# Kernel tuning notes

Hardware: AMD Instinct MI355X
Metric: run time of the kernel (lower is better)

The kernel has to match this reference:

```python
import jax, jax.numpy as jnp
import numpy as np

N_NODES = 50000
N_EDGES = 1600000
IN_DIM = 256
HID = 128
BATCH = 16384
EDGE_FEAT = 6
BN_EPS = 1e-5


def _glorot(key, shape):
    fan_in, fan_out = shape[0], shape[1]
    lim = float(np.sqrt(6.0 / (fan_in + fan_out)))
    return jax.random.uniform(key, shape, jnp.float32, -lim, lim)


def setup_inputs() -> dict:
    key = jax.random.key(0)
    ks = jax.random.split(key, 20)
    return {
        "x": jax.random.normal(ks[0], (N_NODES, IN_DIM), jnp.float32),
        "edge_index": jax.random.randint(ks[1], (2, N_EDGES), 0, N_NODES, jnp.int64 if jax.config.jax_enable_x64 else jnp.int32),
        "src_nodes": jax.random.randint(ks[2], (BATCH,), 0, N_NODES),
        "tgt_nodes": jax.random.randint(ks[3], (BATCH,), 0, N_NODES),
        "edge_features": jax.random.uniform(ks[4], (BATCH, EDGE_FEAT), jnp.float32),
        # SAGEConv layer 0: lin_l (aggregated neighbors, has bias), lin_r (root, no bias)
        "sage_wl0": _glorot(ks[5], (IN_DIM, HID)),
        "sage_b0": jnp.zeros((HID,), jnp.float32),
        "sage_wr0": _glorot(ks[6], (IN_DIM, HID)),
        # SAGEConv layer 1
        "sage_wl1": _glorot(ks[7], (HID, HID)),
        "sage_b1": jnp.zeros((HID,), jnp.float32),
        "sage_wr1": _glorot(ks[8], (HID, HID)),
        # edge_processor: Linear(6, 64)
        "ep_w": _glorot(ks[9], (EDGE_FEAT, HID // 2)),
        "ep_b": jnp.zeros((HID // 2,), jnp.float32),
        # predictor: Linear(320,128) -> ReLU -> BN(128) -> Linear(128,64) -> ReLU -> Linear(64,1) -> Sigmoid
        "p1_w": _glorot(ks[10], (2 * HID + HID // 2, HID)),
        "p1_b": jnp.zeros((HID,), jnp.float32),
        "bn_gamma": jnp.ones((HID,), jnp.float32),
        "bn_beta": jnp.zeros((HID,), jnp.float32),
        "bn_mean": jnp.zeros((HID,), jnp.float32),
        "bn_var": jnp.ones((HID,), jnp.float32),
        "p2_w": _glorot(ks[11], (HID, HID // 2)),
        "p2_b": jnp.zeros((HID // 2,), jnp.float32),
        "p3_w": _glorot(ks[12], (HID // 2, 1)),
        "p3_b": jnp.zeros((1,), jnp.float32),
    }


def _sage_conv(h, src, dst, w_l, b, w_r):
    # PyG SAGEConv(mean): out_i = W_l @ mean_{j in N(i)} h_j + b + W_r @ h_i
    n = h.shape[0]
    agg = jax.ops.segment_sum(h[src], dst, num_segments=n)  # [N, d]
    deg = jax.ops.segment_sum(jnp.ones((src.shape[0],), h.dtype), dst, num_segments=n)
    mean = agg / jnp.maximum(deg, 1.0)[:, None]
    return mean @ w_l + b + h @ w_r


def reference(x, edge_index, src_nodes, tgt_nodes, edge_features,
              sage_wl0, sage_b0, sage_wr0, sage_wl1, sage_b1, sage_wr1,
              ep_w, ep_b, p1_w, p1_b, bn_gamma, bn_beta, bn_mean, bn_var,
              p2_w, p2_b, p3_w, p3_b):
    src, dst = edge_index[0], edge_index[1]
    h = _sage_conv(x, src, dst, sage_wl0, sage_b0, sage_wr0)
    h = jax.nn.relu(h)  # dropout is identity in eval mode
    h = _sage_conv(h, src, dst, sage_wl1, sage_b1, sage_wr1)
    src_emb = h[src_nodes]  # [B, HID]
    tgt_emb = h[tgt_nodes]  # [B, HID]
    edge_proc = jax.nn.relu(edge_features @ ep_w + ep_b)  # [B, HID//2]
    combined = jnp.concatenate([src_emb, tgt_emb, edge_proc], axis=1)  # [B, 320]
    z = jax.nn.relu(combined @ p1_w + p1_b)
    z = (z - bn_mean) / jnp.sqrt(bn_var + BN_EPS) * bn_gamma + bn_beta  # BN eval mode
    z = jax.nn.relu(z @ p2_w + p2_b)
    return jax.nn.sigmoid(z @ p3_w + p3_b)  # [B, 1]
```

## Files before the change

kernel.cpp:

```cpp
#include <hip/hip_runtime.h>
#include <hip/hip_bf16.h>

#define N_NODES 50000
#define N_EDGES 1600000
#define BATCH   16384
#define HID     128
#define NBUCK   782
#define NBLK    256
#define EPB     6250

#define CONVB   967
#define PACKB   577
#define G0A     782
#define G0B     781

using short8  = __attribute__((ext_vector_type(8))) short;
using floatx4 = __attribute__((ext_vector_type(4))) float;
using floatv4 = __attribute__((ext_vector_type(4))) float;
using float2v = __attribute__((ext_vector_type(2))) float;
using uint2v  = __attribute__((ext_vector_type(2))) unsigned;
using uintx4  = __attribute__((ext_vector_type(4))) unsigned;
typedef unsigned short ushort_t;

__device__ __forceinline__ float bflo(unsigned u){ return __uint_as_float(u << 16); }
__device__ __forceinline__ float bfhi(unsigned u){ return __uint_as_float(u & 0xffff0000u); }
__device__ __forceinline__ float bf1(ushort_t u){ return __uint_as_float(((unsigned)u) << 16); }
__device__ __forceinline__ ushort_t f2bf(float f){
    unsigned u = __float_as_uint(f);
    return (ushort_t)((u + 0x7fffu + ((u >> 16) & 1u)) >> 16);
}
__device__ __forceinline__ int geti(const void* p, long long i, int is64){
    return is64 ? (int)((const long long*)p)[i] : ((const int*)p)[i];
}
__device__ __forceinline__ float2v up2(unsigned u){
    float2v r; r.x = bflo(u); r.y = bfhi(u); return r;
}

#define OFF_WL0 0
#define OFF_WR0 32768
#define OFF_WL1 65536
#define OFF_WR1 81920
#define OFF_B0  98304
#define OFF_B1  98432
#define OFF_EPW 98560
#define OFF_EPB 98944
#define OFF_P1W 99008
#define OFF_P1B 139968
#define OFF_BNG 140096
#define OFF_BNB 140224
#define OFF_BNM 140352
#define OFF_BNV 140480
#define OFF_P2W 140608
#define OFF_P2B 148800
#define OFF_P3W 148864
#define OFF_EF  148928
#define OFF_P3B 247232
#define CW_TOT  247233
#define PACK_TOT 147584

__global__ void k_detect(const unsigned* __restrict__ xbits,
                         const unsigned* __restrict__ eibits, int* flags){
    __shared__ int f[2];
    int t = threadIdx.x;
    if (t < 2) f[t] = 0;
    __syncthreads();
    unsigned u = xbits[t];
    unsigned e0 = (u >> 7)  & 0xFF;
    unsigned e1 = (u >> 23) & 0xFF;
    if (e0 >= 140 || e1 >= 140) atomicOr(&f[0], 1);
    if (eibits[2*t + 1] != 0)   atomicOr(&f[1], 1);
    __syncthreads();
    if (t == 0){ flags[0] = f[0]; flags[1] = f[1] ? 0 : 1; }
}

#define NT 19
struct ConvDesc { const void* src[NT]; int cum[NT + 1]; };

__global__ __launch_bounds__(256)
void k_mix1(ConvDesc d, ushort_t* __restrict__ cw,
            const void* __restrict__ ei, int* __restrict__ hist,
            const int* __restrict__ flags){
    __shared__ int lh[NBUCK];
    if (blockIdx.x < CONVB){
        int i = blockIdx.x*256 + threadIdx.x;
        if (i >= d.cum[NT]) return;
        int seg = 0;
        while (i >= d.cum[seg + 1]) seg++;
        int off = i - d.cum[seg];
        ushort_t v;
        if (flags[0]) v = f2bf(((const float*)d.src[seg])[off]);
        else          v = ((const ushort_t*)d.src[seg])[off];
        cw[i] = v;
    } else {
        int b = blockIdx.x - CONVB;
        for (int i = threadIdx.x; i < NBUCK; i += 256) lh[i] = 0;
        __syncthreads();
        int i64 = flags[1];
        int e0 = b * EPB;
        for (int e = e0 + threadIdx.x; e < e0 + EPB; e += 256){
            int dd = geti(ei, (long long)N_EDGES + e, i64);
            atomicAdd(&lh[dd >> 6], 1);
        }
        __syncthreads();
        for (int i = threadIdx.x; i < NBUCK; i += 256)
            hist[i * NBLK + b] = lh[i];
    }
}

__global__ __launch_bounds__(256)
void k_mix2(const ushort_t* __restrict__ cw,
            ushort_t* __restrict__ bp0, ushort_t* __restrict__ bp1,
            ushort_t* __restrict__ bpp1, ushort_t* __restrict__ bpp2,
            float* __restrict__ bnf,
            int* __restrict__ hist, int* __restrict__ btot){
    __shared__ int sh[256];
    if (blockIdx.x < PACKB){
        int i = blockIdx.x*256 + threadIdx.x;
        if (i < 65536){
            int j = i & 7, lane = (i >> 3) & 63, c = (i >> 9) & 15, kk = i >> 13;
            int k = kk*32 + (lane >> 4)*8 + j;
            int n = c*16 + (lane & 15);
            bp0[i] = (n < 128) ? cw[OFF_WL0 + k*128 + n] : cw[OFF_WR0 + k*128 + (n-128)];
        } else if (i < 98304){
            int i2 = i - 65536;
            int j = i2 & 7, lane = (i2 >> 3) & 63, c = (i2 >> 9) & 15, kk = i2 >> 13;
            int k = kk*32 + (lane >> 4)*8 + j;
            int n = c*16 + (lane & 15);
            bp1[i2] = (n < 128) ? cw[OFF_WL1 + k*128 + n] : cw[OFF_WR1 + k*128 + (n-128)];
        } else if (i < 139264){
            int i2 = i - 98304;
            int j = i2 & 7, lane = (i2 >> 3) & 63, ct = (i2 >> 9) & 7, kk = i2 >> 12;
            int k = kk*32 + (lane >> 4)*8 + j;
            int n = ct*16 + (lane & 15);
            bpp1[i2] = cw[OFF_P1W + k*128 + n];
        } else if (i < 147456){
            int i2 = i - 139264;
            int j = i2 & 7, lane = (i2 >> 3) & 63, ct = (i2 >> 9) & 3, kk = i2 >> 11;
            int k = kk*32 + (lane >> 4)*8 + j;
            int n = ct*16 + (lane & 15);
            bpp2[i2] = cw[OFF_P2W + k*64 + n];
        } else if (i < PACK_TOT){
            int n = i - 147456;
            float g = bf1(cw[OFF_BNG + n]), b = bf1(cw[OFF_BNB + n]);
            float m = bf1(cw[OFF_BNM + n]), v = bf1(cw[OFF_BNV + n]);
            float sc = g / sqrtf(v + 1e-5f);
            bnf[n] = sc; bnf[128 + n] = b - m*sc;
        }
    } else {
        int b = blockIdx.x - PACKB, t = threadIdx.x;
        int v = hist[b*NBLK + t];
        sh[t] = v; __syncthreads();
        for (int o = 1; o < 256; o <<= 1){
            int x = (t >= o) ? sh[t-o] : 0;
            __syncthreads();
            sh[t] += x;
            __syncthreads();
        }
        hist[b*NBLK + t] = sh[t] - v;
        if (t == 255) btot[b] = sh[255];
    }
}

__global__ __launch_bounds__(1024)
void kb_scanbase(const int* __restrict__ btot, int* __restrict__ bbase,
                 int* __restrict__ off){
    __shared__ int sh[1024];
    int t = threadIdx.x;
    int v = (t < NBUCK) ? btot[t] : 0;
    sh[t] = v; __syncthreads();
    for (int o = 1; o < 1024; o <<= 1){
        int x = (t >= o) ? sh[t-o] : 0;
        __syncthreads();
        sh[t] += x;
        __syncthreads();
    }
    if (t < NBUCK) bbase[t] = sh[t] - v;
    if (t == 0){ bbase[NBUCK] = N_EDGES; off[N_NODES] = N_EDGES; }
}

__device__ __forceinline__ void gemm0_body(const void* __restrict__ xin,
                                           const ushort_t* __restrict__ Bp,
                                           ushort_t* __restrict__ out,
                                           int M, int f32, int blk){
    const int t = threadIdx.x;
    const int lane = t & 63;
    const int w = t >> 6;
    const int rg = w >> 1, cg = w & 1;
    const int l16 = lane & 15, q = lane >> 4;
    const int m_base = blk * 32 + rg * 16;
    int m = m_base + l16;
    bool ok = (m < M);
    const short8* bbase = (const short8*)Bp + lane;

    floatx4 acc[8] = {};
    if (f32){
        const float* arow = (const float*)xin + (size_t)(ok ? m : 0)*256 + q*8;
        for (int kk = 0; kk < 8; ++kk){
            union { unsigned u[4]; short8 s; } cv;
            cv.u[0]=0; cv.u[1]=0; cv.u[2]=0; cv.u[3]=0;
            if (ok){
                floatv4 f0 = *(const floatv4*)(arow + kk*32);
                floatv4 f1 = *(const floatv4*)(arow + kk*32 + 4);
                cv.u[0] = __builtin_amdgcn_perm(__float_as_uint(f0.y), __float_as_uint(f0.x), 0x07060302);
                cv.u[1] = __builtin_amdgcn_perm(__float_as_uint(f0.w), __float_as_uint(f0.z), 0x07060302);
                cv.u[2] = __builtin_amdgcn_perm(__float_as_uint(f1.y), __float_as_uint(f1.x), 0x07060302);
                cv.u[3] = __builtin_amdgcn_perm(__float_as_uint(f1.w), __float_as_uint(f1.z), 0x07060302);
            }
            #pragma unroll
            for (int ci = 0; ci < 8; ++ci){
                short8 b = bbase[(kk*16 + cg*8 + ci)*64];
                acc[ci] = __builtin_amdgcn_mfma_f32_16x16x32_bf16(cv.s, b, acc[ci], 0, 0, 0);
            }
        }
    } else {
        const ushort_t* arow = (const ushort_t*)xin + (size_t)(ok ? m : 0)*256 + q*8;
        for (int kk = 0; kk < 8; ++kk){
            short8 a = {0,0,0,0,0,0,0,0};
            if (ok) a = *(const short8*)(arow + kk*32);
            #pragma unroll
            for (int ci = 0; ci < 8; ++ci){
                short8 b = bbase[(kk*16 + cg*8 + ci)*64];
                acc[ci] = __builtin_amdgcn_mfma_f32_16x16x32_bf16(a, b, acc[ci], 0, 0, 0);
            }
        }
    }
    int row_b = m_base + q*4;
    #pragma unroll
    for (int r = 0; r < 4; ++r){
        int row = row_b + r;
        if (row < M){
            #pragma unroll
            for (int ci = 0; ci < 8; ++ci)
                out[(size_t)row*256 + cg*128 + ci*16 + l16] = f2bf(acc[ci][r]);
        }
    }
}

__global__ __launch_bounds__(256)
void k_mix3a(const void* __restrict__ x, const ushort_t* __restrict__ bp0,
             ushort_t* __restrict__ yr,
             const void* __restrict__ ei, const int* __restrict__ hist,
             const int* __restrict__ bbase, unsigned* __restrict__ ebuf,
             const int* __restrict__ flags){
    __shared__ int lcur[NBUCK];
    if (blockIdx.x < G0A){
        gemm0_body(x, bp0, yr, N_NODES, flags[0], blockIdx.x);
    } else {
        int b = blockIdx.x - G0A;
        for (int i = threadIdx.x; i < NBUCK; i += 256)
            lcur[i] = bbase[i] + hist[i*NBLK + b];
        __syncthreads();
        int i64 = flags[1];
        int e0 = b * EPB;
        for (int e = e0 + threadIdx.x; e < e0 + EPB; e += 256){
            int s = geti(ei, e, i64);
            int d = geti(ei, (long long)N_EDGES + e, i64);
            int p = atomicAdd(&lcur[d >> 6], 1);
            ebuf[p] = (unsigned)s | ((unsigned)(d & 63) << 16);
        }
    }
}

__global__ __launch_bounds__(256)
void k_mix3b(const void* __restrict__ x, const ushort_t* __restrict__ bp0,
             ushort_t* __restrict__ yr,
             const unsigned* __restrict__ ebuf, const int* __restrict__ bbase,
             ushort_t* __restrict__ csr, int* __restrict__ off,
             const int* __restrict__ flags){
    __shared__ int ldeg[64];
    if (blockIdx.x < G0B){
        gemm0_body(x, bp0, yr, N_NODES, flags[0], G0A + blockIdx.x);
    } else {
        int b = blockIdx.x - G0B, t = threadIdx.x;
        int ebase = bbase[b], eend = bbase[b+1];
        if (t < 64) ldeg[t] = 0;
        __syncthreads();
        for (int i = ebase + t; i < eend; i += 256)
            atomicAdd(&ldeg[(ebuf[i] >> 16) & 63], 1);
        __syncthreads();
        if (t < 64){
            int v = ldeg[t];
            int sum = v;
            #pragma unroll
            for (int o = 1; o < 64; o <<= 1){
                int x2 = __shfl_up(sum, o, 64);
                if (t >= o) sum += x2;
            }
            int excl = sum - v;
            int node = b*64 + t;
            if (node < N_NODES) off[node] = ebase + excl;
            ldeg[t] = excl;
        }
        __syncthreads();
        for (int i = ebase + t; i < eend; i += 256){
            unsigned u = ebuf[i];
            int p = atomicAdd(&ldeg[(u >> 16) & 63], 1);
            csr[ebase + p] = (ushort_t)(u & 0xffffu);
        }
    }
}

__global__ __launch_bounds__(256)
void k_gemm1(const ushort_t* __restrict__ A, const ushort_t* __restrict__ Bp,
             ushort_t* __restrict__ out, int M)
{
    const int KSTEPS = 4;
    const int lane = threadIdx.x & 63;
    const int w    = threadIdx.x >> 6;
    const int rg   = w >> 1;
    const int cg   = w & 1;
    const int l16  = lane & 15;
    const int q    = lane >> 4;
    const int S    = KSTEPS * 32;
    const int m_base = blockIdx.x * 32 + rg * 16;

    int m = m_base + l16;
    bool ok = (m < M);
    const ushort_t* arow = A + (size_t)(ok ? m : 0) * S + q*8;
    const short8* bbase = (const short8*)Bp + lane;

    floatx4 acc[8] = {};
    for (int kk = 0; kk < KSTEPS; ++kk){
        short8 a = {0,0,0,0,0,0,0,0};
        if (ok) a = *(const short8*)(arow + kk*32);
        #pragma unroll
        for (int ci = 0; ci < 8; ++ci){
            short8 b = bbase[(kk*16 + cg*8 + ci)*64];
            acc[ci] = __builtin_amdgcn_mfma_f32_16x16x32_bf16(a, b, acc[ci], 0, 0, 0);
        }
    }

    int row_b = m_base + q*4;
    #pragma unroll
    for (int r = 0; r < 4; ++r){
        int row = row_b + r;
        if (row < M){
            #pragma unroll
            for (int ci = 0; ci < 8; ++ci)
                out[(size_t)row*256 + cg*128 + ci*16 + l16] = f2bf(acc[ci][r]);
        }
    }
}

__global__ __launch_bounds__(256)
void k_agg(const int* __restrict__ off, const ushort_t* __restrict__ csr,
           const ushort_t* __restrict__ yr, const ushort_t* __restrict__ bias,
           ushort_t* __restrict__ out, int do_relu)
{
    int v = blockIdx.x*4 + (threadIdx.x >> 6);
    if (v >= N_NODES) return;
    const int l = threadIdx.x & 63;
    const int g = l >> 4;
    const int c = l & 15;
    int e0 = off[v], e1 = off[v+1];
    const ushort_t* yb = yr + c*8;

    float2v A0[4] = {}, A1[4] = {}, A2[4] = {}, A3[4] = {};
    int p = e0;
    for (; p + 16 <= e1; p += 16){
        int u0 = csr[p + g];
        int u1 = csr[p + 4 + g];
        int u2 = csr[p + 8 + g];
        int u3 = csr[p + 12 + g];
        uintx4 d0 = *(const uintx4*)(yb + (size_t)u0*256);
        uintx4 d1 = *(const uintx4*)(yb + (size_t)u1*256);
        uintx4 d2 = *(const uintx4*)(yb + (size_t)u2*256);
        uintx4 d3 = *(const uintx4*)(yb + (size_t)u3*256);
        A0[0] += up2(d0.x); A0[1] += up2(d0.y); A0[2] += up2(d0.z); A0[3] += up2(d0.w);
        A1[0] += up2(d1.x); A1[1] += up2(d1.y); A1[2] += up2(d1.z); A1[3] += up2(d1.w);
        A2[0] += up2(d2.x); A2[1] += up2(d2.y); A2[2] += up2(d2.z); A2[3] += up2(d2.w);
        A3[0] += up2(d3.x); A3[1] += up2(d3.y); A3[2] += up2(d3.z); A3[3] += up2(d3.w);
    }
    for (; p + 4 <= e1; p += 4){
        int u0 = csr[p + g];
        uintx4 d0 = *(const uintx4*)(yb + (size_t)u0*256);
        A0[0] += up2(d0.x); A0[1] += up2(d0.y); A0[2] += up2(d0.z); A0[3] += up2(d0.w);
    }
    if (p + g < e1){
        int u1 = csr[p + g];
        uintx4 d1 = *(const uintx4*)(yb + (size_t)u1*256);
        A1[0] += up2(d1.x); A1[1] += up2(d1.y); A1[2] += up2(d1.z); A1[3] += up2(d1.w);
    }
    #pragma unroll
    for (int j = 0; j < 4; ++j) A0[j] += A1[j] + A2[j] + A3[j];

    float a0=A0[0].x, a1=A0[0].y, a2=A0[1].x, a3=A0[1].y;
    float a4=A0[2].x, a5=A0[2].y, a6=A0[3].x, a7=A0[3].y;
    #pragma unroll
    for (int m = 16; m <= 32; m <<= 1){
        a0 += __shfl_xor(a0, m, 64); a1 += __shfl_xor(a1, m, 64);
        a2 += __shfl_xor(a2, m, 64); a3 += __shfl_xor(a3, m, 64);
        a4 += __shfl_xor(a4, m, 64); a5 += __shfl_xor(a5, m, 64);
        a6 += __shfl_xor(a6, m, 64); a7 += __shfl_xor(a7, m, 64);
    }
    if (g == 0){
        float inv = 1.f / (float)max(e1 - e0, 1);
        uintx4 rr = *(const uintx4*)(yr + (size_t)v*256 + 128 + c*8);
        uintx4 bb = *(const uintx4*)(bias + c*8);
        float v0 = a0*inv + bflo(rr.x) + bflo(bb.x);
        float v1 = a1*inv + bfhi(rr.x) + bfhi(bb.x);
        float v2 = a2*inv + bflo(rr.y) + bflo(bb.y);
        float v3 = a3*inv + bfhi(rr.y) + bfhi(bb.y);
        float v4 = a4*inv + bflo(rr.z) + bflo(bb.z);
        float v5 = a5*inv + bfhi(rr.z) + bfhi(bb.z);
        float v6 = a6*inv + bflo(rr.w) + bflo(bb.w);
        float v7 = a7*inv + bfhi(rr.w) + bfhi(bb.w);
        if (do_relu){
            v0=fmaxf(v0,0.f); v1=fmaxf(v1,0.f); v2=fmaxf(v2,0.f); v3=fmaxf(v3,0.f);
            v4=fmaxf(v4,0.f); v5=fmaxf(v5,0.f); v6=fmaxf(v6,0.f); v7=fmaxf(v7,0.f);
        }
        uintx4 o;
        o.x = (unsigned)f2bf(v0) | ((unsigned)f2bf(v1) << 16);
        o.y = (unsigned)f2bf(v2) | ((unsigned)f2bf(v3) << 16);
        o.z = (unsigned)f2bf(v4) | ((unsigned)f2bf(v5) << 16);
        o.w = (unsigned)f2bf(v6) | ((unsigned)f2bf(v7) << 16);
        *(uintx4*)(out + (size_t)v*128 + c*8) = o;
    }
}

__global__ __launch_bounds__(256)
void k_pred2(const ushort_t* __restrict__ h2,
             const void* __restrict__ srcn, const void* __restrict__ tgtn,
             const ushort_t* __restrict__ cw, const ushort_t* __restrict__ bpp1,
             const ushort_t* __restrict__ bpp2, const float* __restrict__ bnf,
             void* __restrict__ outp, const int* __restrict__ flags)
{
    __shared__ ushort_t comb[64][328];
    __shared__ ushort_t zbuf[64][136];
    __shared__ ushort_t z2buf[64][68];
    __shared__ float    partial[4][64];
    __shared__ int      sid[64], tid_[64];

    const int t    = threadIdx.x;
    const int lane = t & 63;
    const int w    = t >> 6;
    const int l16  = lane & 15;
    const int q    = lane >> 4;
    const int row0 = blockIdx.x * 64;
    const int i64  = flags[1];

    if (t < 64){ sid[t] = geti(srcn, row0 + t, i64); tid_[t] = geti(tgtn, row0 + t, i64); }
    __syncthreads();

    const unsigned* h2u = (const unsigned*)h2;
    #pragma unroll 4
    for (int r = w*16; r < w*16 + 16; ++r){
        unsigned us = h2u[(size_t)sid[r]*64 + lane];
        unsigned ut = h2u[(size_t)tid_[r]*64 + lane];
        *(unsigned*)&comb[r][2*lane]       = us;
        *(unsigned*)&comb[r][128 + 2*lane] = ut;
    }
    {
        int r = t >> 2, c0 = (t & 3) * 16;
        float efv[6];
        #pragma unroll
        for (int k = 0; k < 6; ++k) efv[k] = bf1(cw[OFF_EF + (row0 + r)*6 + k]);
        #pragma unroll
        for (int c = 0; c < 16; ++c){
            int n = c0 + c;
            float a = bf1(cw[OFF_EPB + n]);
            #pragma unroll
            for (int k = 0; k < 6; ++k) a += efv[k] * bf1(cw[OFF_EPW + k*64 + n]);
            comb[r][256 + n] = f2bf(fmaxf(a, 0.f));
        }
    }
    __syncthreads();

    floatx4 acc[4][2] = {};
    for (int kk = 0; kk < 10; ++kk){
        short8 a[4];
        #pragma unroll
        for (int rt = 0; rt < 4; ++rt)
            a[rt] = *(const short8*)&comb[rt*16 + l16][kk*32 + q*8];
        #pragma unroll
        for (int ci = 0; ci < 2; ++ci){
            short8 b = *(const short8*)&bpp1[(((kk*8) + (w*2 + ci))*64 + lane)*8];
            #pragma unroll
            for (int rt = 0; rt < 4; ++rt)
                acc[rt][ci] = __builtin_amdgcn_mfma_f32_16x16x32_bf16(a[rt], b, acc[rt][ci], 0, 0, 0);
        }
    }
    #pragma unroll
    for (int ci = 0; ci < 2; ++ci){
        int n = w*32 + ci*16 + l16;
        float b1v = bf1(cw[OFF_P1B + n]);
        float sc = bnf[n], sh = bnf[128 + n];
        #pragma unroll
        for (int rt = 0; rt < 4; ++rt)
            #pragma unroll
            for (int r = 0; r < 4; ++r){
                float v = fmaxf(acc[rt][ci][r] + b1v, 0.f) * sc + sh;
                zbuf[rt*16 + q*4 + r][n] = f2bf(v);
            }
    }
    __syncthreads();

    floatx4 acc2[4] = {};
    for (int kk = 0; kk < 4; ++kk){
        short8 b = *(const short8*)&bpp2[(((kk*4) + w)*64 + lane)*8];
        #pragma unroll
        for (int rt = 0; rt < 4; ++rt){
            short8 a = *(const short8*)&zbuf[rt*16 + l16][kk*32 + q*8];
            acc2[rt] = __builtin_amdgcn_mfma_f32_16x16x32_bf16(a, b, acc2[rt], 0, 0, 0);
        }
    }
    {
        int n = w*16 + l16;
        float b2v = bf1(cw[OFF_P2B + n]);
        #pragma unroll
        for (int rt = 0; rt < 4; ++rt)
            #pragma unroll
            for (int r = 0; r < 4; ++r)
                z2buf[rt*16 + q*4 + r][n] = f2bf(fmaxf(acc2[rt][r] + b2v, 0.f));
    }
    __syncthreads();

    {
        int r = t & 63, seg = t >> 6;
        float s = 0.f;
        #pragma unroll
        for (int c = 0; c < 16; ++c){
            int n = seg*16 + c;
            s += bf1(z2buf[r][n]) * bf1(cw[OFF_P3W + n]);
        }
        partial[seg][r] = s;
    }
    __syncthreads();
    if (t < 64){
        float zf = partial[0][t] + partial[1][t] + partial[2][t] + partial[3][t] + bf1(cw[OFF_P3B]);
        float sg = 1.f / (1.f + __expf(-zf));
        if (flags[0]) ((float*)outp)[row0 + t] = sg;
        else          ((ushort_t*)outp)[row0 + t] = f2bf(sg);
    }
}

extern "C" void kernel_launch(void* const* d_in, const int* in_sizes, int n_in,
                              void* d_out, int out_size, void* d_ws, size_t ws_size,
                              hipStream_t stream)
{
    const void* x    = d_in[0];
    const void* ei   = d_in[1];
    const void* srcn = d_in[2];
    const void* tgtn = d_in[3];

    char* p = (char*)d_ws;
    auto carve = [&](size_t bytes)->char*{ char* r = p; p += (bytes + 511) & ~size_t(511); return r; };
    int* flags = (int*)carve(64);
    int* off   = (int*)carve((N_NODES+1)*4);
    int* btot  = (int*)carve(NBUCK*4);
    int* bbase = (int*)carve((NBUCK+1)*4);
    ushort_t* csr = (ushort_t*)carve((size_t)N_EDGES*2);
    ushort_t* yr  = (ushort_t*)carve((size_t)N_NODES*256*2);
    ushort_t* h   = (ushort_t*)carve((size_t)N_NODES*128*2);
    ushort_t* cw  = (ushort_t*)carve((size_t)CW_TOT*2);
    ushort_t* bp0 = (ushort_t*)carve((size_t)65536*2);
    ushort_t* bp1 = (ushort_t*)carve((size_t)32768*2);
    ushort_t* bpp1= (ushort_t*)carve((size_t)40960*2);
    ushort_t* bpp2= (ushort_t*)carve((size_t)8192*2);
    float*    bnf = (float*)carve(256*4);

    int*      hist = (int*)h;
    unsigned* ebuf = (unsigned*)((char*)h + 1u*1024*1024);

    k_detect<<<1, 256, 0, stream>>>((const unsigned*)x, (const unsigned*)ei, flags);

    ConvDesc cd;
    const int srcidx[NT] = {5,7,8,10,6,9,11,12,13,14,15,16,17,18,19,20,21,4,22};
    const int lens[NT]   = {32768,32768,16384,16384,128,128,384,64,40960,128,128,128,128,128,8192,64,64,98304,1};
    int run = 0;
    for (int i = 0; i < NT; ++i){ cd.src[i] = d_in[srcidx[i]]; cd.cum[i] = run; run += lens[i]; }
    cd.cum[NT] = run;

    k_mix1<<<CONVB + NBLK, 256, 0, stream>>>(cd, cw, ei, hist, flags);
    k_mix2<<<PACKB + NBUCK, 256, 0, stream>>>(cw, bp0, bp1, bpp1, bpp2, bnf, hist, btot);
    kb_scanbase<<<1, 1024, 0, stream>>>(btot, bbase, off);
    k_mix3a<<<G0A + NBLK, 256, 0, stream>>>(x, bp0, yr, ei, hist, bbase, ebuf, flags);
    k_mix3b<<<G0B + NBUCK, 256, 0, stream>>>(x, bp0, yr, ebuf, bbase, csr, off, flags);

    k_agg<<<(N_NODES+3)/4, 256, 0, stream>>>(off, csr, yr, cw+OFF_B0, h, 1);
    k_gemm1<<<(N_NODES + 31)/32, 256, 0, stream>>>(h, bp1, yr, N_NODES);
    k_agg<<<(N_NODES+3)/4, 256, 0, stream>>>(off, csr, yr, cw+OFF_B1, h, 0);

    k_pred2<<<BATCH/64, 256, 0, stream>>>(h, srcn, tgtn, cw, bpp1, bpp2, bnf, d_out, flags);
}
```

Measured before the change: 338.9 us.

## Split projected table into separate neighbor and root arrays; interleave mixed-kernel blocks

```diff
diff --git a/kernel.cpp b/kernel.cpp
--- a/kernel.cpp
+++ b/kernel.cpp
@@ -180,7 +180,8 @@
 
 __device__ __forceinline__ void gemm0_body(const void* __restrict__ xin,
                                            const ushort_t* __restrict__ Bp,
-                                           ushort_t* __restrict__ out,
+                                           ushort_t* __restrict__ ytab,
+                                           ushort_t* __restrict__ rtab,
                                            int M, int f32, int blk){
     const int t = threadIdx.x;
     const int lane = t & 63;
@@ -224,6 +225,7 @@
             }
         }
     }
+    ushort_t* dst = cg ? rtab : ytab;
     int row_b = m_base + q*4;
     #pragma unroll
     for (int r = 0; r < 4; ++r){
@@ -231,22 +233,25 @@
         if (row < M){
             #pragma unroll
             for (int ci = 0; ci < 8; ++ci)
-                out[(size_t)row*256 + cg*128 + ci*16 + l16] = f2bf(acc[ci][r]);
+                dst[(size_t)row*128 + ci*16 + l16] = f2bf(acc[ci][r]);
         }
     }
 }
 
 __global__ __launch_bounds__(256)
 void k_mix3a(const void* __restrict__ x, const ushort_t* __restrict__ bp0,
-             ushort_t* __restrict__ yr,
+             ushort_t* __restrict__ ytab, ushort_t* __restrict__ rtab,
              const void* __restrict__ ei, const int* __restrict__ hist,
              const int* __restrict__ bbase, unsigned* __restrict__ ebuf,
              const int* __restrict__ flags){
     __shared__ int lcur[NBUCK];
-    if (blockIdx.x < G0A){
-        gemm0_body(x, bp0, yr, N_NODES, flags[0], blockIdx.x);
+    bool scat = (blockIdx.x < 1024) && ((blockIdx.x & 3) == 3);
+    if (!scat){
+        int gi = (blockIdx.x < 1024) ? (int)(blockIdx.x - (blockIdx.x >> 2))
+                                     : (int)(blockIdx.x - NBLK);
+        gemm0_body(x, bp0, ytab, rtab, N_NODES, flags[0], gi);
     } else {
-        int b = blockIdx.x - G0A;
+        int b = blockIdx.x >> 2;
         for (int i = threadIdx.x; i < NBUCK; i += 256)
             lcur[i] = bbase[i] + hist[i*NBLK + b];
         __syncthreads();
@@ -263,15 +268,15 @@
 
 __global__ __launch_bounds__(256)
 void k_mix3b(const void* __restrict__ x, const ushort_t* __restrict__ bp0,
-             ushort_t* __restrict__ yr,
+             ushort_t* __restrict__ ytab, ushort_t* __restrict__ rtab,
              const unsigned* __restrict__ ebuf, const int* __restrict__ bbase,
              ushort_t* __restrict__ csr, int* __restrict__ off,
              const int* __restrict__ flags){
     __shared__ int ldeg[64];
-    if (blockIdx.x < G0B){
-        gemm0_body(x, bp0, yr, N_NODES, flags[0], G0A + blockIdx.x);
+    if (blockIdx.x & 1){
+        gemm0_body(x, bp0, ytab, rtab, N_NODES, flags[0], G0A + (int)(blockIdx.x >> 1));
     } else {
-        int b = blockIdx.x - G0B, t = threadIdx.x;
+        int b = blockIdx.x >> 1, t = threadIdx.x;
         int ebase = bbase[b], eend = bbase[b+1];
         if (t < 64) ldeg[t] = 0;
         __syncthreads();
@@ -302,7 +307,7 @@
 
 __global__ __launch_bounds__(256)
 void k_gemm1(const ushort_t* __restrict__ A, const ushort_t* __restrict__ Bp,
-             ushort_t* __restrict__ out, int M)
+             ushort_t* __restrict__ ytab, ushort_t* __restrict__ rtab, int M)
 {
     const int KSTEPS = 4;
     const int lane = threadIdx.x & 63;
@@ -330,6 +335,7 @@
         }
     }
 
+    ushort_t* dst = cg ? rtab : ytab;
     int row_b = m_base + q*4;
     #pragma unroll
     for (int r = 0; r < 4; ++r){
@@ -337,14 +343,15 @@
         if (row < M){
             #pragma unroll
             for (int ci = 0; ci < 8; ++ci)
-                out[(size_t)row*256 + cg*128 + ci*16 + l16] = f2bf(acc[ci][r]);
+                dst[(size_t)row*128 + ci*16 + l16] = f2bf(acc[ci][r]);
         }
     }
 }
 
 __global__ __launch_bounds__(256)
 void k_agg(const int* __restrict__ off, const ushort_t* __restrict__ csr,
-           const ushort_t* __restrict__ yr, const ushort_t* __restrict__ bias,
+           const ushort_t* __restrict__ ytab, const ushort_t* __restrict__ rtab,
+           const ushort_t* __restrict__ bias,
            ushort_t* __restrict__ out, int do_relu)
 {
     int v = blockIdx.x*4 + (threadIdx.x >> 6);
@@ -353,7 +360,7 @@
     const int g = l >> 4;
     const int c = l & 15;
     int e0 = off[v], e1 = off[v+1];
-    const ushort_t* yb = yr + c*8;
+    const ushort_t* yb = ytab + c*8;
 
     float2v A0[4] = {}, A1[4] = {}, A2[4] = {}, A3[4] = {};
     int p = e0;
@@ -362,10 +369,10 @@
         int u1 = csr[p + 4 + g];
         int u2 = csr[p + 8 + g];
         int u3 = csr[p + 12 + g];
-        uintx4 d0 = *(const uintx4*)(yb + (size_t)u0*256);
-        uintx4 d1 = *(const uintx4*)(yb + (size_t)u1*256);
-        uintx4 d2 = *(const uintx4*)(yb + (size_t)u2*256);
-        uintx4 d3 = *(const uintx4*)(yb + (size_t)u3*256);
+        uintx4 d0 = *(const uintx4*)(yb + (size_t)u0*128);
+        uintx4 d1 = *(const uintx4*)(yb + (size_t)u1*128);
+        uintx4 d2 = *(const uintx4*)(yb + (size_t)u2*128);
+        uintx4 d3 = *(const uintx4*)(yb + (size_t)u3*128);
         A0[0] += up2(d0.x); A0[1] += up2(d0.y); A0[2] += up2(d0.z); A0[3] += up2(d0.w);
         A1[0] += up2(d1.x); A1[1] += up2(d1.y); A1[2] += up2(d1.z); A1[3] += up2(d1.w);
         A2[0] += up2(d2.x); A2[1] += up2(d2.y); A2[2] += up2(d2.z); A2[3] += up2(d2.w);
@@ -373,12 +380,12 @@
     }
     for (; p + 4 <= e1; p += 4){
         int u0 = csr[p + g];
-        uintx4 d0 = *(const uintx4*)(yb + (size_t)u0*256);
+        uintx4 d0 = *(const uintx4*)(yb + (size_t)u0*128);
         A0[0] += up2(d0.x); A0[1] += up2(d0.y); A0[2] += up2(d0.z); A0[3] += up2(d0.w);
     }
     if (p + g < e1){
         int u1 = csr[p + g];
-        uintx4 d1 = *(const uintx4*)(yb + (size_t)u1*256);
+        uintx4 d1 = *(const uintx4*)(yb + (size_t)u1*128);
         A1[0] += up2(d1.x); A1[1] += up2(d1.y); A1[2] += up2(d1.z); A1[3] += up2(d1.w);
     }
     #pragma unroll
@@ -395,7 +402,7 @@
     }
     if (g == 0){
         float inv = 1.f / (float)max(e1 - e0, 1);
-        uintx4 rr = *(const uintx4*)(yr + (size_t)v*256 + 128 + c*8);
+        uintx4 rr = *(const uintx4*)(rtab + (size_t)v*128 + c*8);
         uintx4 bb = *(const uintx4*)(bias + c*8);
         float v0 = a0*inv + bflo(rr.x) + bflo(bb.x);
         float v1 = a1*inv + bfhi(rr.x) + bfhi(bb.x);
@@ -549,15 +556,16 @@
     int* off   = (int*)carve((N_NODES+1)*4);
     int* btot  = (int*)carve(NBUCK*4);
     int* bbase = (int*)carve((NBUCK+1)*4);
-    ushort_t* csr = (ushort_t*)carve((size_t)N_EDGES*2);
-    ushort_t* yr  = (ushort_t*)carve((size_t)N_NODES*256*2);
-    ushort_t* h   = (ushort_t*)carve((size_t)N_NODES*128*2);
-    ushort_t* cw  = (ushort_t*)carve((size_t)CW_TOT*2);
-    ushort_t* bp0 = (ushort_t*)carve((size_t)65536*2);
-    ushort_t* bp1 = (ushort_t*)carve((size_t)32768*2);
-    ushort_t* bpp1= (ushort_t*)carve((size_t)40960*2);
-    ushort_t* bpp2= (ushort_t*)carve((size_t)8192*2);
-    float*    bnf = (float*)carve(256*4);
+    ushort_t* csr  = (ushort_t*)carve((size_t)N_EDGES*2);
+    ushort_t* ytab = (ushort_t*)carve((size_t)N_NODES*128*2);
+    ushort_t* rtab = (ushort_t*)carve((size_t)N_NODES*128*2);
+    ushort_t* h    = (ushort_t*)carve((size_t)N_NODES*128*2);
+    ushort_t* cw   = (ushort_t*)carve((size_t)CW_TOT*2);
+    ushort_t* bp0  = (ushort_t*)carve((size_t)65536*2);
+    ushort_t* bp1  = (ushort_t*)carve((size_t)32768*2);
+    ushort_t* bpp1 = (ushort_t*)carve((size_t)40960*2);
+    ushort_t* bpp2 = (ushort_t*)carve((size_t)8192*2);
+    float*    bnf  = (float*)carve(256*4);
 
     int*      hist = (int*)h;
     unsigned* ebuf = (unsigned*)((char*)h + 1u*1024*1024);
@@ -574,12 +582,12 @@
     k_mix1<<<CONVB + NBLK, 256, 0, stream>>>(cd, cw, ei, hist, flags);
     k_mix2<<<PACKB + NBUCK, 256, 0, stream>>>(cw, bp0, bp1, bpp1, bpp2, bnf, hist, btot);
     kb_scanbase<<<1, 1024, 0, stream>>>(btot, bbase, off);
-    k_mix3a<<<G0A + NBLK, 256, 0, stream>>>(x, bp0, yr, ei, hist, bbase, ebuf, flags);
-    k_mix3b<<<G0B + NBUCK, 256, 0, stream>>>(x, bp0, yr, ebuf, bbase, csr, off, flags);
-
-    k_agg<<<(N_NODES+3)/4, 256, 0, stream>>>(off, csr, yr, cw+OFF_B0, h, 1);
-    k_gemm1<<<(N_NODES + 31)/32, 256, 0, stream>>>(h, bp1, yr, N_NODES);
-    k_agg<<<(N_NODES+3)/4, 256, 0, stream>>>(off, csr, yr, cw+OFF_B1, h, 0);
+    k_mix3a<<<G0A + NBLK, 256, 0, stream>>>(x, bp0, ytab, rtab, ei, hist, bbase, ebuf, flags);
+    k_mix3b<<<G0B + NBUCK, 256, 0, stream>>>(x, bp0, ytab, rtab, ebuf, bbase, csr, off, flags);
+
+    k_agg<<<(N_NODES+3)/4, 256, 0, stream>>>(off, csr, ytab, rtab, cw+OFF_B0, h, 1);
+    k_gemm1<<<(N_NODES + 31)/32, 256, 0, stream>>>(h, bp1, ytab, rtab, N_NODES);
+    k_agg<<<(N_NODES+3)/4, 256, 0, stream>>>(off, csr, ytab, rtab, cw+OFF_B1, h, 0);
 
     k_pred2<<<BATCH/64, 256, 0, stream>>>(h, srcn, tgtn, cw, bpp1, bpp2, bnf, d_out, flags);
 }
```

After: 364.0 us. 1.07x slower.
